# Optimization experiments

Measured on AMD Instinct MI355X. Metric: run time of the kernel, lower is better.

## Reference

```python
import jax, jax.numpy as jnp
import numpy as np

N_NODES = 100000


def gcn_conv(x, src, dst, W, b, n_nodes):
    # x: [N, Fin], src/dst: [E'] (self-loops already included)
    h = x @ W  # [N, Fout] transform first (Fout <= Fin friendly)
    ones = jnp.ones(src.shape[0], dtype=x.dtype)
    deg = jax.ops.segment_sum(ones, dst, num_segments=n_nodes)  # in-degree with self-loops
    dinv = jnp.where(deg > 0, jax.lax.rsqrt(deg), 0.0)
    norm = dinv[src] * dinv[dst]  # [E']
    msg = h[src] * norm[:, None]  # gather + scale
    out = jax.ops.segment_sum(msg, dst, num_segments=n_nodes)  # scatter-add
    return out + b


def setup_inputs() -> dict:
    key = jax.random.key(0)
    ks = jax.random.split(key, 5)
    n, e, fin, hid, ncls = N_NODES, 3200000, 128, 64, 11
    x = jax.random.normal(ks[0], (n, fin), dtype=jnp.float32)
    edge_index = jax.random.randint(ks[1], (2, e), 0, n, dtype=jnp.int64)
    W1 = jax.random.normal(ks[2], (fin, hid), dtype=jnp.float32) * (1.0 / np.sqrt(fin))
    b1 = jnp.zeros((hid,), dtype=jnp.float32)
    W2 = jax.random.normal(ks[3], (hid, hid), dtype=jnp.float32) * (1.0 / np.sqrt(hid))
    b2 = jnp.zeros((hid,), dtype=jnp.float32)
    Wfc = jax.random.normal(ks[4], (hid, ncls), dtype=jnp.float32) * (1.0 / np.sqrt(hid))
    bfc = jnp.zeros((ncls,), dtype=jnp.float32)
    return {"x": x, "edge_index": edge_index, "W1": W1, "b1": b1,
            "W2": W2, "b2": b2, "Wfc": Wfc, "bfc": bfc}


def reference(x, edge_index, W1, b1, W2, b2, Wfc, bfc):
    n = x.shape[0]
    loops = jnp.arange(n, dtype=edge_index.dtype)
    src = jnp.concatenate([edge_index[0], loops])  # add self-loops (GCNConv default)
    dst = jnp.concatenate([edge_index[1], loops])
    h = gcn_conv(x, src, dst, W1, b1, n)
    h = jax.nn.relu(h)  # dropout is identity in eval mode
    h = gcn_conv(h, src, dst, W2, b2, n)
    h = jax.nn.relu(h)
    return h @ Wfc + bfc
```

## Files before the change

### kernel.cpp

```cpp
#include <hip/hip_runtime.h>
#include <hip/hip_fp16.h>

#define HID 64
#define SH 9
#define BKN 512
#define MAXB1 256
#define NBLK 512
typedef unsigned int u32;
typedef float f32x4 __attribute__((ext_vector_type(4)));
typedef _Float16 f16x4 __attribute__((ext_vector_type(4)));
typedef _Float16 f16x8 __attribute__((ext_vector_type(8)));

__global__ __launch_bounds__(256) void count_chunks(const int* __restrict__ dst,
                                                    int* __restrict__ cnt2,
                                                    int E, int nbk) {
  __shared__ int lc[MAXB1];
  const int t = threadIdx.x;
  for (int b = t; b < nbk; b += 256) lc[b] = 0;
  __syncthreads();
  const int C = (E + NBLK - 1) / NBLK;
  const int s0 = blockIdx.x * C;
  const int s1 = min(s0 + C, E);
  for (int i = s0 + t; i < s1; i += 256) atomicAdd(&lc[dst[i] >> SH], 1);
  __syncthreads();
  for (int b = t; b < nbk; b += 256)
    cnt2[(size_t)b * NBLK + blockIdx.x] = lc[b];
}

__global__ __launch_bounds__(256) void scan_blocks(const int* __restrict__ v_in,
                                                   int* __restrict__ excl,
                                                   int* __restrict__ bsum, int n) {
  __shared__ int s[256];
  const int t = threadIdx.x;
  const int i = blockIdx.x * 256 + t;
  const int v = (i < n) ? v_in[i] : 0;
  s[t] = v;
  __syncthreads();
  for (int off = 1; off < 256; off <<= 1) {
    const int u = (t >= off) ? s[t - off] : 0;
    __syncthreads();
    s[t] += u;
    __syncthreads();
  }
  if (i < n) excl[i] = s[t] - v;
  if (t == 255) bsum[blockIdx.x] = s[255];
}

__global__ __launch_bounds__(512) void scan_top(int* bsum, int nb) {
  __shared__ int s[512];
  const int t = threadIdx.x;
  const int v = (t < nb) ? bsum[t] : 0;
  s[t] = v;
  __syncthreads();
  for (int off = 1; off < 512; off <<= 1) {
    const int u = (t >= off) ? s[t - off] : 0;
    __syncthreads();
    s[t] += u;
    __syncthreads();
  }
  if (t < nb) bsum[t] = s[t] - v;
}

__global__ __launch_bounds__(256) void add_offsets2(int* __restrict__ off,
                                                    const int* __restrict__ bsum,
                                                    int* __restrict__ boff,
                                                    int NE, int E, int nbk) {
  const int m = blockIdx.x * 256 + threadIdx.x;
  if (m < NE) {
    const int v = off[m] + bsum[blockIdx.x];
    off[m] = v;
    if ((m & (NBLK - 1)) == 0) boff[m >> 9] = v;
  }
  if (m == 0) boff[nbk] = E;
}

__global__ __launch_bounds__(512) void fill_pairs(const int* __restrict__ src,
                                                  const int* __restrict__ dst,
                                                  const int* __restrict__ off,
                                                  u32* __restrict__ pairs,
                                                  int E, int nbk) {
  __shared__ int lbase[MAXB1];
  __shared__ int lrank[MAXB1];
  const int t = threadIdx.x;
  for (int b = t; b < nbk; b += 512) {
    lbase[b] = off[(size_t)b * NBLK + blockIdx.x];
    lrank[b] = 0;
  }
  __syncthreads();
  const int C = (E + NBLK - 1) / NBLK;
  const int s0 = blockIdx.x * C;
  const int s1 = min(s0 + C, E);
  for (int i = s0 + t; i < s1; i += 512) {
    const int d = dst[i];
    const int b = d >> SH;
    const int r = atomicAdd(&lrank[b], 1);
    pairs[lbase[b] + r] = ((u32)(d & (BKN - 1)) << 17) | (u32)src[i];
  }
}

__global__ __launch_bounds__(1024) void bucket_csr(const u32* __restrict__ pairs,
                                                   const int* __restrict__ boff,
                                                   int* __restrict__ rowptr,
                                                   int* __restrict__ rowend,
                                                   float* __restrict__ dinv,
                                                   int* __restrict__ colidx,
                                                   int n, int nbk) {
  __shared__ int ldeg[BKN];
  __shared__ int lofs[BKN];
  const int bkt = blockIdx.x;
  const int t = threadIdx.x;
  if (t < BKN) ldeg[t] = 0;
  __syncthreads();
  const int beg = boff[bkt], end = boff[bkt + 1];
  const int cnt = end - beg;
  for (int e = t; e < cnt; e += 1024)
    atomicAdd(&ldeg[pairs[beg + e] >> 17], 1);
  __syncthreads();
  const int node = bkt * BKN + t;
  int dg = 0, pdg = 0;
  if (t < BKN) {
    dg = ldeg[t];
    pdg = (node < n) ? ((dg + 1 + 7) & ~7) : 0;
    lofs[t] = pdg;
  }
  __syncthreads();
  for (int o = 1; o < BKN; o <<= 1) {
    int u = 0;
    if (t < BKN && t >= o) u = lofs[t - o];
    __syncthreads();
    if (t < BKN) lofs[t] += u;
    __syncthreads();
  }
  const int pbase = beg + bkt * (BKN * 8);
  if (t < BKN && node < n) {
    const int base = pbase + lofs[t] - pdg;
    rowptr[node] = base;
    rowend[node] = base + pdg;
    dinv[node] = rsqrtf((float)(dg + 1));
    colidx[base] = node;
    for (int j = 1 + dg; j < pdg; ++j) colidx[base + j] = n;
    ldeg[t] = base + 1;
  }
  __syncthreads();
  for (int e = t; e < cnt; e += 1024) {
    const u32 p = pairs[beg + e];
    const int pos = atomicAdd(&ldeg[p >> 17], 1);
    colidx[pos] = (int)(p & 0x1FFFF);
  }
}

__global__ __launch_bounds__(256) void gemm1_mfma(const float* __restrict__ x,
                                                  const float* __restrict__ W,
                                                  const float* __restrict__ dinv,
                                                  __half* __restrict__ out, int n) {
  __shared__ _Float16 Ah[64 * 136];
  __shared__ _Float16 Wt[64 * 136];
  const int tid = threadIdx.x;
  const int row0 = blockIdx.x * 64;
  for (int i = tid; i < 64 * 32; i += 256) {
    const int r = i >> 5, q = i & 31;
    const int gr = row0 + r;
    float4 v = {0.f, 0.f, 0.f, 0.f};
    if (gr < n) v = reinterpret_cast<const float4*>(x)[(size_t)gr * 32 + q];
    f16x4 hv = {(_Float16)v.x, (_Float16)v.y, (_Float16)v.z, (_Float16)v.w};
    *reinterpret_cast<f16x4*>(&Ah[r * 136 + q * 4]) = hv;
  }
  for (int i = tid; i < 64 * 32; i += 256) {
    const int c = i & 63, k0 = (i >> 6) * 4;
    f16x4 hv = {(_Float16)W[(size_t)(k0 + 0) * 64 + c],
                (_Float16)W[(size_t)(k0 + 1) * 64 + c],
                (_Float16)W[(size_t)(k0 + 2) * 64 + c],
                (_Float16)W[(size_t)(k0 + 3) * 64 + c]};
    *reinterpret_cast<f16x4*>(&Wt[c * 136 + k0]) = hv;
  }
  __syncthreads();
  const int lane = tid & 63;
  const int m = lane & 15, g = lane >> 4;
  const int r0 = (tid >> 6) * 16;
  f32x4 acc0 = {0.f, 0.f, 0.f, 0.f}, acc1 = acc0, acc2 = acc0, acc3 = acc0;
  const _Float16* arow = &Ah[(r0 + m) * 136];
#pragma unroll
  for (int kc = 0; kc < 4; ++kc) {
    const int ko = kc * 32 + g * 4;
    const f16x4 alo = *reinterpret_cast<const f16x4*>(arow + ko);
    const f16x4 ahi = *reinterpret_cast<const f16x4*>(arow + ko + 16);
    const f16x8 a = __builtin_shufflevector(alo, ahi, 0, 1, 2, 3, 4, 5, 6, 7);
    const f16x4 bl0 = *reinterpret_cast<const f16x4*>(&Wt[(0  + m) * 136 + ko]);
    const f16x4 bh0 = *reinterpret_cast<const f16x4*>(&Wt[(0  + m) * 136 + ko + 16]);
    const f16x4 bl1 = *reinterpret_cast<const f16x4*>(&Wt[(16 + m) * 136 + ko]);
    const f16x4 bh1 = *reinterpret_cast<const f16x4*>(&Wt[(16 + m) * 136 + ko + 16]);
    const f16x4 bl2 = *reinterpret_cast<const f16x4*>(&Wt[(32 + m) * 136 + ko]);
    const f16x4 bh2 = *reinterpret_cast<const f16x4*>(&Wt[(32 + m) * 136 + ko + 16]);
    const f16x4 bl3 = *reinterpret_cast<const f16x4*>(&Wt[(48 + m) * 136 + ko]);
    const f16x4 bh3 = *reinterpret_cast<const f16x4*>(&Wt[(48 + m) * 136 + ko + 16]);
    const f16x8 b0 = __builtin_shufflevector(bl0, bh0, 0, 1, 2, 3, 4, 5, 6, 7);
    const f16x8 b1 = __builtin_shufflevector(bl1, bh1, 0, 1, 2, 3, 4, 5, 6, 7);
    const f16x8 b2 = __builtin_shufflevector(bl2, bh2, 0, 1, 2, 3, 4, 5, 6, 7);
    const f16x8 b3 = __builtin_shufflevector(bl3, bh3, 0, 1, 2, 3, 4, 5, 6, 7);
    acc0 = __builtin_amdgcn_mfma_f32_16x16x32_f16(a, b0, acc0, 0, 0, 0);
    acc1 = __builtin_amdgcn_mfma_f32_16x16x32_f16(a, b1, acc1, 0, 0, 0);
    acc2 = __builtin_amdgcn_mfma_f32_16x16x32_f16(a, b2, acc2, 0, 0, 0);
    acc3 = __builtin_amdgcn_mfma_f32_16x16x32_f16(a, b3, acc3, 0, 0, 0);
  }
  _Float16* o16 = reinterpret_cast<_Float16*>(out);
#pragma unroll
  for (int j = 0; j < 4; ++j) {
    const int grow = row0 + r0 + g * 4 + j;
    if (grow < n) {
      const float di = dinv[grow];
      o16[(size_t)grow * 64 + 0  + m] = (_Float16)(acc0[j] * di);
      o16[(size_t)grow * 64 + 16 + m] = (_Float16)(acc1[j] * di);
      o16[(size_t)grow * 64 + 32 + m] = (_Float16)(acc2[j] * di);
      o16[(size_t)grow * 64 + 48 + m] = (_Float16)(acc3[j] * di);
    }
  }
}

__global__ __launch_bounds__(256) void gemm2_mfma(const __half* __restrict__ h,
                                                  const float* __restrict__ W,
                                                  const float* __restrict__ dinv,
                                                  __half* __restrict__ out, int n) {
  __shared__ _Float16 Ah[64 * 72];
  __shared__ _Float16 Wt[64 * 72];
  const int tid = threadIdx.x;
  const int row0 = blockIdx.x * 64;
  for (int i = tid; i < 64 * 8; i += 256) {
    const int r = i >> 3, q = i & 7;
    const int gr = row0 + r;
    float4 raw = {0.f, 0.f, 0.f, 0.f};
    if (gr < n) raw = reinterpret_cast<const float4*>(h)[(size_t)gr * 8 + q];
    *reinterpret_cast<float4*>(&Ah[r * 72 + q * 8]) = raw;
  }
  for (int i = tid; i < 64 * 16; i += 256) {
    const int c = i & 63, k0 = (i >> 6) * 4;
    f16x4 hv = {(_Float16)W[(size_t)(k0 + 0) * 64 + c],
                (_Float16)W[(size_t)(k0 + 1) * 64 + c],
                (_Float16)W[(size_t)(k0 + 2) * 64 + c],
                (_Float16)W[(size_t)(k0 + 3) * 64 + c]};
    *reinterpret_cast<f16x4*>(&Wt[c * 72 + k0]) = hv;
  }
  __syncthreads();
  const int lane = tid & 63;
  const int m = lane & 15, g = lane >> 4;
  const int r0 = (tid >> 6) * 16;
  f32x4 acc0 = {0.f, 0.f, 0.f, 0.f}, acc1 = acc0, acc2 = acc0, acc3 = acc0;
  const _Float16* arow = &Ah[(r0 + m) * 72];
#pragma unroll
  for (int kc = 0; kc < 2; ++kc) {
    const int ko = kc * 32 + g * 4;
    const f16x4 alo = *reinterpret_cast<const f16x4*>(arow + ko);
    const f16x4 ahi = *reinterpret_cast<const f16x4*>(arow + ko + 16);
    const f16x8 a = __builtin_shufflevector(alo, ahi, 0, 1, 2, 3, 4, 5, 6, 7);
    const f16x4 bl0 = *reinterpret_cast<const f16x4*>(&Wt[(0  + m) * 72 + ko]);
    const f16x4 bh0 = *reinterpret_cast<const f16x4*>(&Wt[(0  + m) * 72 + ko + 16]);
    const f16x4 bl1 = *reinterpret_cast<const f16x4*>(&Wt[(16 + m) * 72 + ko]);
    const f16x4 bh1 = *reinterpret_cast<const f16x4*>(&Wt[(16 + m) * 72 + ko + 16]);
    const f16x4 bl2 = *reinterpret_cast<const f16x4*>(&Wt[(32 + m) * 72 + ko]);
    const f16x4 bh2 = *reinterpret_cast<const f16x4*>(&Wt[(32 + m) * 72 + ko + 16]);
    const f16x4 bl3 = *reinterpret_cast<const f16x4*>(&Wt[(48 + m) * 72 + ko]);
    const f16x4 bh3 = *reinterpret_cast<const f16x4*>(&Wt[(48 + m) * 72 + ko + 16]);
    const f16x8 b0 = __builtin_shufflevector(bl0, bh0, 0, 1, 2, 3, 4, 5, 6, 7);
    const f16x8 b1 = __builtin_shufflevector(bl1, bh1, 0, 1, 2, 3, 4, 5, 6, 7);
    const f16x8 b2 = __builtin_shufflevector(bl2, bh2, 0, 1, 2, 3, 4, 5, 6, 7);
    const f16x8 b3 = __builtin_shufflevector(bl3, bh3, 0, 1, 2, 3, 4, 5, 6, 7);
    acc0 = __builtin_amdgcn_mfma_f32_16x16x32_f16(a, b0, acc0, 0, 0, 0);
    acc1 = __builtin_amdgcn_mfma_f32_16x16x32_f16(a, b1, acc1, 0, 0, 0);
    acc2 = __builtin_amdgcn_mfma_f32_16x16x32_f16(a, b2, acc2, 0, 0, 0);
    acc3 = __builtin_amdgcn_mfma_f32_16x16x32_f16(a, b3, acc3, 0, 0, 0);
  }
  _Float16* o16 = reinterpret_cast<_Float16*>(out);
#pragma unroll
  for (int j = 0; j < 4; ++j) {
    const int grow = row0 + r0 + g * 4 + j;
    if (grow < n) {
      const float di = dinv[grow];
      o16[(size_t)grow * 64 + 0  + m] = (_Float16)(acc0[j] * di);
      o16[(size_t)grow * 64 + 16 + m] = (_Float16)(acc1[j] * di);
      o16[(size_t)grow * 64 + 32 + m] = (_Float16)(acc2[j] * di);
      o16[(size_t)grow * 64 + 48 + m] = (_Float16)(acc3[j] * di);
    }
  }
}

__global__ __launch_bounds__(256) void gather_agg(const int* __restrict__ rowptr,
                                                  const int* __restrict__ rowend,
                                                  const int* __restrict__ colidx,
                                                  const __half2* __restrict__ g2,
                                                  const float* __restrict__ dinv,
                                                  const float* __restrict__ bias,
                                                  __half2* __restrict__ outp, int n) {
  const int lane = threadIdx.x & 63;
  const int node = (blockIdx.x * 256 + threadIdx.x) >> 6;
  if (node >= n) return;
  const int h = lane >> 5;
  const int l = lane & 31;
  const int beg = rowptr[node];
  const int end = rowend[node];
  float2 acc = {0.f, 0.f};
  int e = beg + h;
  for (; e + 30 < end; e += 32) {
    int s[16];
#pragma unroll
    for (int j = 0; j < 16; ++j) s[j] = colidx[e + 2 * j];
    float2 v[16];
#pragma unroll
    for (int j = 0; j < 16; ++j)
      v[j] = __half22float2(g2[((u32)s[j] << 5) + (u32)l]);
#pragma unroll
    for (int j = 0; j < 16; ++j) {
      acc.x += v[j].x;
      acc.y += v[j].y;
    }
  }
  for (; e + 6 < end; e += 8) {
    const int s0 = colidx[e + 0], s1 = colidx[e + 2];
    const int s2 = colidx[e + 4], s3 = colidx[e + 6];
    const float2 v0 = __half22float2(g2[((u32)s0 << 5) + (u32)l]);
    const float2 v1 = __half22float2(g2[((u32)s1 << 5) + (u32)l]);
    const float2 v2 = __half22float2(g2[((u32)s2 << 5) + (u32)l]);
    const float2 v3 = __half22float2(g2[((u32)s3 << 5) + (u32)l]);
    acc.x += (v0.x + v1.x) + (v2.x + v3.x);
    acc.y += (v0.y + v1.y) + (v2.y + v3.y);
  }
  acc.x += __shfl_xor(acc.x, 32);
  acc.y += __shfl_xor(acc.y, 32);
  const float di = dinv[node];
  const float2 bb = reinterpret_cast<const float2*>(bias)[l];
  const float rx = fmaxf(fmaf(acc.x, di, bb.x), 0.f);
  const float ry = fmaxf(fmaf(acc.y, di, bb.y), 0.f);
  if (h == 0) outp[(size_t)node * 32 + l] = __floats2half2_rn(rx, ry);
}

__global__ __launch_bounds__(256) void gemm_fc(const __half* __restrict__ h,
                                               const float* __restrict__ W,
                                               const float* __restrict__ b,
                                               float* __restrict__ out, int n) {
  __shared__ float Wl[772];
  __shared__ float xl[16][68];
  const int tid = threadIdx.x;
  for (int i = tid; i < 772; i += 256) Wl[i] = 0.f;
  __syncthreads();
  for (int i = tid; i < 64 * 11; i += 256) Wl[(i / 11) * 12 + (i % 11)] = W[i];
  const int row00 = blockIdx.x * 64;
  for (int rr = 0; rr < 4; ++rr) {
    const int row0 = row00 + rr * 16;
    __syncthreads();
    if (tid < 128) {
      const int r = tid >> 3, q = tid & 7;
      const int grow = row0 + r;
      if (grow < n) {
        const float4 hv = *reinterpret_cast<const float4*>(
            h + (size_t)grow * 64 + q * 8);
        const __half2* hp = reinterpret_cast<const __half2*>(&hv);
#pragma unroll
        for (int j = 0; j < 4; ++j) {
          const float2 f = __half22float2(hp[j]);
          xl[r][q * 8 + 2 * j + 0] = f.x;
          xl[r][q * 8 + 2 * j + 1] = f.y;
        }
      }
    }
    __syncthreads();
    const int r = tid >> 4, c = tid & 15;
    float acc = 0.f;
#pragma unroll
    for (int k = 0; k < 64; k += 4) {
      acc = fmaf(xl[r][k + 0], Wl[(k + 0) * 12 + c], acc);
      acc = fmaf(xl[r][k + 1], Wl[(k + 1) * 12 + c], acc);
      acc = fmaf(xl[r][k + 2], Wl[(k + 2) * 12 + c], acc);
      acc = fmaf(xl[r][k + 3], Wl[(k + 3) * 12 + c], acc);
    }
    const int grow = row0 + r;
    if (c < 11 && grow < n) out[(size_t)grow * 11 + c] = acc + b[c];
  }
}

extern "C" void kernel_launch(void* const* d_in, const int* in_sizes, int n_in,
                              void* d_out, int out_size, void* d_ws, size_t ws_size,
                              hipStream_t stream) {
  const float* x   = (const float*)d_in[0];
  const int*   ei  = (const int*)d_in[1];
  const float* W1  = (const float*)d_in[2];
  const float* b1  = (const float*)d_in[3];
  const float* W2  = (const float*)d_in[4];
  const float* b2  = (const float*)d_in[5];
  const float* Wfc = (const float*)d_in[6];
  const float* bfc = (const float*)d_in[7];
  float* out = (float*)d_out;

  const int n = in_sizes[0] / 128;
  const int E = in_sizes[1] / 2;
  const int* src = ei;
  const int* dst = ei + E;
  const int nbk = (n + BKN - 1) >> SH;
  const int NE = nbk * NBLK;

  char* ws = (char*)d_ws;
  size_t o = 0;
  auto alloc = [&](size_t bytes) {
    char* p = ws + o;
    o += (bytes + 255) & ~(size_t)255;
    return p;
  };
  float*  dinv   = (float*) alloc((size_t)n * 4);
  int*    rowptr = (int*)   alloc((size_t)n * 4);
  int*    rowend = (int*)   alloc((size_t)n * 4);
  int*    cnt2   = (int*)   alloc((size_t)NE * 4);
  int*    off    = (int*)   alloc((size_t)NE * 4);
  int*    bsum2  = (int*)   alloc(512 * 4);
  int*    boff   = (int*)   alloc((size_t)(nbk + 1) * 4);
  u32*    pairs  = (u32*)   alloc((size_t)E * 4);
  int*    colidx = (int*)   alloc(((size_t)E + (size_t)nbk * BKN * 8) * 4);
  __half* B0h    = (__half*)alloc((size_t)(n + 1) * HID * 2);
  __half* B1h    = (__half*)alloc((size_t)n * HID * 2);
  if (o > ws_size) return;

  const int nb2 = (NE + 255) / 256;
  const int gblocks = (n + 63) / 64;
  const int fcblocks = (n + 63) / 64;

  hipMemsetAsync(B0h + (size_t)n * HID, 0, HID * 2, stream);

  count_chunks<<<NBLK, 256, 0, stream>>>(dst, cnt2, E, nbk);
  scan_blocks<<<nb2, 256, 0, stream>>>(cnt2, off, bsum2, NE);
  scan_top<<<1, 512, 0, stream>>>(bsum2, nb2);
  add_offsets2<<<nb2, 256, 0, stream>>>(off, bsum2, boff, NE, E, nbk);
  fill_pairs<<<NBLK, 512, 0, stream>>>(src, dst, off, pairs, E, nbk);
  bucket_csr<<<nbk, 1024, 0, stream>>>(pairs, boff, rowptr, rowend, dinv,
                                       colidx, n, nbk);

  const int pull_blocks = (n * 64 + 255) / 256;

  gemm1_mfma<<<gblocks, 256, 0, stream>>>(x, W1, dinv, B0h, n);
  gather_agg<<<pull_blocks, 256, 0, stream>>>(rowptr, rowend, colidx,
      (const __half2*)B0h, dinv, b1, (__half2*)B1h, n);

  gemm2_mfma<<<gblocks, 256, 0, stream>>>(B1h, W2, dinv, B0h, n);
  gather_agg<<<pull_blocks, 256, 0, stream>>>(rowptr, rowend, colidx,
      (const __half2*)B0h, dinv, b2, (__half2*)B1h, n);

  gemm_fc<<<fcblocks, 256, 0, stream>>>(B1h, Wfc, bfc, out, n);
}
```

Measured before the change: 219.3 us.

## Fold offset-add kernel into consumers, vectorize edge loads, warp-shuffle bucket scan

Removes the add_offsets2 kernel: fill_pairs and bucket_csr now add the block sums to the per-chunk scan values on the fly, which saves one launch and a read/write pass over the offset array. count_chunks and fill_pairs read dst/src as int4 with chunk sizes rounded to multiples of 4, to cut load instructions. bucket_csr replaces its shared-memory Hillis-Steele scan, which needed many __syncthreads, with a wavefront shuffle scan followed by a small cross-wave prefix. The int4 loads assume the edge arrays are 16-byte aligned and that E is a multiple of 4 (true for 3.2M edges); otherwise the vector loads near the end can read past the array.

```diff
diff --git a/kernel.cpp b/kernel.cpp
--- a/kernel.cpp
+++ b/kernel.cpp
@@ -11,6 +11,10 @@
 typedef _Float16 f16x4 __attribute__((ext_vector_type(4)));
 typedef _Float16 f16x8 __attribute__((ext_vector_type(8)));
 
+__device__ __forceinline__ int chunk4(int E) {
+  return (((E + NBLK - 1) / NBLK) + 3) & ~3;
+}
+
 __global__ __launch_bounds__(256) void count_chunks(const int* __restrict__ dst,
                                                     int* __restrict__ cnt2,
                                                     int E, int nbk) {
@@ -18,10 +22,16 @@
   const int t = threadIdx.x;
   for (int b = t; b < nbk; b += 256) lc[b] = 0;
   __syncthreads();
-  const int C = (E + NBLK - 1) / NBLK;
+  const int C = chunk4(E);
   const int s0 = blockIdx.x * C;
   const int s1 = min(s0 + C, E);
-  for (int i = s0 + t; i < s1; i += 256) atomicAdd(&lc[dst[i] >> SH], 1);
+  for (int i = s0 + t * 4; i < s1; i += 1024) {
+    const int4 d4 = *reinterpret_cast<const int4*>(&dst[i]);
+    atomicAdd(&lc[d4.x >> SH], 1);
+    atomicAdd(&lc[d4.y >> SH], 1);
+    atomicAdd(&lc[d4.z >> SH], 1);
+    atomicAdd(&lc[d4.w >> SH], 1);
+  }
   __syncthreads();
   for (int b = t; b < nbk; b += 256)
     cnt2[(size_t)b * NBLK + blockIdx.x] = lc[b];
@@ -61,79 +71,99 @@
   if (t < nb) bsum[t] = s[t] - v;
 }
 
-__global__ __launch_bounds__(256) void add_offsets2(int* __restrict__ off,
-                                                    const int* __restrict__ bsum,
-                                                    int* __restrict__ boff,
-                                                    int NE, int E, int nbk) {
-  const int m = blockIdx.x * 256 + threadIdx.x;
-  if (m < NE) {
-    const int v = off[m] + bsum[blockIdx.x];
-    off[m] = v;
-    if ((m & (NBLK - 1)) == 0) boff[m >> 9] = v;
-  }
-  if (m == 0) boff[nbk] = E;
-}
-
 __global__ __launch_bounds__(512) void fill_pairs(const int* __restrict__ src,
                                                   const int* __restrict__ dst,
                                                   const int* __restrict__ off,
+                                                  const int* __restrict__ bsum2,
                                                   u32* __restrict__ pairs,
                                                   int E, int nbk) {
   __shared__ int lbase[MAXB1];
   __shared__ int lrank[MAXB1];
   const int t = threadIdx.x;
+  const int blk = blockIdx.x;
   for (int b = t; b < nbk; b += 512) {
-    lbase[b] = off[(size_t)b * NBLK + blockIdx.x];
+    const int m = b * NBLK + blk;
+    lbase[b] = off[m] + bsum2[m >> 8];
     lrank[b] = 0;
   }
   __syncthreads();
-  const int C = (E + NBLK - 1) / NBLK;
-  const int s0 = blockIdx.x * C;
+  const int C = chunk4(E);
+  const int s0 = blk * C;
   const int s1 = min(s0 + C, E);
-  for (int i = s0 + t; i < s1; i += 512) {
-    const int d = dst[i];
-    const int b = d >> SH;
-    const int r = atomicAdd(&lrank[b], 1);
-    pairs[lbase[b] + r] = ((u32)(d & (BKN - 1)) << 17) | (u32)src[i];
+  for (int i = s0 + t * 4; i < s1; i += 2048) {
+    const int4 d4 = *reinterpret_cast<const int4*>(&dst[i]);
+    const int4 v4 = *reinterpret_cast<const int4*>(&src[i]);
+    {
+      const int b = d4.x >> SH;
+      const int r = atomicAdd(&lrank[b], 1);
+      pairs[lbase[b] + r] = ((u32)(d4.x & (BKN - 1)) << 17) | (u32)v4.x;
+    }
+    {
+      const int b = d4.y >> SH;
+      const int r = atomicAdd(&lrank[b], 1);
+      pairs[lbase[b] + r] = ((u32)(d4.y & (BKN - 1)) << 17) | (u32)v4.y;
+    }
+    {
+      const int b = d4.z >> SH;
+      const int r = atomicAdd(&lrank[b], 1);
+      pairs[lbase[b] + r] = ((u32)(d4.z & (BKN - 1)) << 17) | (u32)v4.z;
+    }
+    {
+      const int b = d4.w >> SH;
+      const int r = atomicAdd(&lrank[b], 1);
+      pairs[lbase[b] + r] = ((u32)(d4.w & (BKN - 1)) << 17) | (u32)v4.w;
+    }
   }
 }
 
 __global__ __launch_bounds__(1024) void bucket_csr(const u32* __restrict__ pairs,
-                                                   const int* __restrict__ boff,
+                                                   const int* __restrict__ off,
+                                                   const int* __restrict__ bsum2,
                                                    int* __restrict__ rowptr,
                                                    int* __restrict__ rowend,
                                                    float* __restrict__ dinv,
                                                    int* __restrict__ colidx,
-                                                   int n, int nbk) {
+                                                   int n, int nbk, int E) {
   __shared__ int ldeg[BKN];
-  __shared__ int lofs[BKN];
+  __shared__ int wsum[8];
+  __shared__ int wexcl[8];
   const int bkt = blockIdx.x;
   const int t = threadIdx.x;
   if (t < BKN) ldeg[t] = 0;
   __syncthreads();
-  const int beg = boff[bkt], end = boff[bkt + 1];
+  const int m0 = bkt * NBLK;
+  const int beg = off[m0] + bsum2[m0 >> 8];
+  const int end = (bkt == nbk - 1)
+                      ? E
+                      : off[m0 + NBLK] + bsum2[(m0 + NBLK) >> 8];
   const int cnt = end - beg;
   for (int e = t; e < cnt; e += 1024)
     atomicAdd(&ldeg[pairs[beg + e] >> 17], 1);
   __syncthreads();
   const int node = bkt * BKN + t;
-  int dg = 0, pdg = 0;
+  const int lane = t & 63, w = t >> 6;
+  int dg = 0, pdg = 0, incl = 0;
   if (t < BKN) {
     dg = ldeg[t];
-    pdg = (node < n) ? ((dg + 1 + 7) & ~7) : 0;
-    lofs[t] = pdg;
-  }
-  __syncthreads();
-  for (int o = 1; o < BKN; o <<= 1) {
-    int u = 0;
-    if (t < BKN && t >= o) u = lofs[t - o];
-    __syncthreads();
-    if (t < BKN) lofs[t] += u;
-    __syncthreads();
-  }
+    pdg = (node < n) ? ((dg + 8) & ~7) : 0;
+    incl = pdg;
+  }
+#pragma unroll
+  for (int o = 1; o < 64; o <<= 1) {
+    const int u = __shfl_up(incl, o);
+    if (lane >= o) incl += u;
+  }
+  if (t < BKN && lane == 63) wsum[w] = incl;
+  __syncthreads();
+  if (t == 0) {
+    int run = 0;
+#pragma unroll
+    for (int i = 0; i < 8; ++i) { wexcl[i] = run; run += wsum[i]; }
+  }
+  __syncthreads();
   const int pbase = beg + bkt * (BKN * 8);
   if (t < BKN && node < n) {
-    const int base = pbase + lofs[t] - pdg;
+    const int base = pbase + wexcl[w] + incl - pdg;
     rowptr[node] = base;
     rowend[node] = base + pdg;
     dinv[node] = rsqrtf((float)(dg + 1));
@@ -408,7 +438,6 @@
   int*    cnt2   = (int*)   alloc((size_t)NE * 4);
   int*    off    = (int*)   alloc((size_t)NE * 4);
   int*    bsum2  = (int*)   alloc(512 * 4);
-  int*    boff   = (int*)   alloc((size_t)(nbk + 1) * 4);
   u32*    pairs  = (u32*)   alloc((size_t)E * 4);
   int*    colidx = (int*)   alloc(((size_t)E + (size_t)nbk * BKN * 8) * 4);
   __half* B0h    = (__half*)alloc((size_t)(n + 1) * HID * 2);
@@ -424,10 +453,9 @@
   count_chunks<<<NBLK, 256, 0, stream>>>(dst, cnt2, E, nbk);
   scan_blocks<<<nb2, 256, 0, stream>>>(cnt2, off, bsum2, NE);
   scan_top<<<1, 512, 0, stream>>>(bsum2, nb2);
-  add_offsets2<<<nb2, 256, 0, stream>>>(off, bsum2, boff, NE, E, nbk);
-  fill_pairs<<<NBLK, 512, 0, stream>>>(src, dst, off, pairs, E, nbk);
-  bucket_csr<<<nbk, 1024, 0, stream>>>(pairs, boff, rowptr, rowend, dinv,
-                                       colidx, n, nbk);
+  fill_pairs<<<NBLK, 512, 0, stream>>>(src, dst, off, bsum2, pairs, E, nbk);
+  bucket_csr<<<nbk, 1024, 0, stream>>>(pairs, off, bsum2, rowptr, rowend, dinv,
+                                       colidx, n, nbk, E);
 
   const int pull_blocks = (n * 64 + 255) / 256;
 
```

Measured after the change: 211.0 us. 3.8% less time.
